# Kernel tuning notes

Hardware: AMD Instinct MI355X
Metric: run time of the kernel (lower is better)

Reference implementation:

```python
import jax, jax.numpy as jnp
import numpy as np

B, K = 2048, 128
M = 5 * K
ALPHA = 1.0 / K          # alpha_k = 1/K
VARTHETA = 0.1
PMAX = 10.0
BIG = 1e9


def _gnn(HW, X, W0a, W1a, W0b, W1b):
    """Order-1 graph filter GNN (HWGCN, K0=[1,1]): relu hidden layer, linear output.
    HW: (B,K,K), X: (B,K,Fin) -> (B,K,Fout)."""
    SX = jnp.einsum('bij,bjf->bif', HW, X)
    Z = jax.nn.relu(X @ W0a + SX @ W1a)              # (B,K,32)
    SZ = jnp.einsum('bij,bjh->bih', HW, Z)
    return Z @ W0b + SZ @ W1b                        # (B,K,Fout)


def setup_inputs() -> dict:
    key = jax.random.key(0)
    ks = jax.random.split(key, 16)
    s = 0.05
    d = {
        'num_itr': 10,
        'kth': 9,
        'HW': jnp.abs(jax.random.normal(ks[0], (B, K, K), jnp.float32)) * s,
        'x0_tmp': jax.random.uniform(ks[1], (B, M), jnp.float32),
        'nu3_val': jnp.array([0.1], jnp.float32),
        'tilde_gamma_val': jnp.array([2.0], jnp.float32),
        'A9': jax.random.normal(ks[2], (1,), jnp.float32),
        'A1': jax.random.normal(ks[3], (1,), jnp.float32),
        'A3': jax.random.normal(ks[4], (1,), jnp.float32),
        'A7': jax.random.normal(ks[5], (1,), jnp.float32),
        'b7': jax.random.normal(ks[6], (1,), jnp.float32),
        'A10': jax.random.normal(ks[7], (1,), jnp.float32),
        'g1_W0a': jax.random.normal(ks[8], (5, 32), jnp.float32) * s,
        'g1_W1a': jax.random.normal(ks[9], (5, 32), jnp.float32) * s,
        'g1_W0b': jax.random.normal(ks[10], (32, 2), jnp.float32) * s,
        'g1_W1b': jax.random.normal(ks[11], (32, 2), jnp.float32) * s,
        'g2_W0a': jax.random.normal(ks[12], (K + 5, 32), jnp.float32) * s,
        'g2_W1a': jax.random.normal(ks[13], (K + 5, 32), jnp.float32) * s,
        'g2_W0b': jax.random.normal(ks[14], (32, 5), jnp.float32) * s,
        'g2_W1b': jax.random.normal(ks[15], (32, 5), jnp.float32) * s,
    }
    return d


def reference(num_itr, kth, HW, x0_tmp, nu3_val, tilde_gamma_val,
              A9, A1, A3, A7, b7, A10,
              g1_W0a, g1_W1a, g1_W0b, g1_W1b,
              g2_W0a, g2_W1a, g2_W0b, g2_W1b):
    nu3 = nu3_val[0]
    tg = tilde_gamma_val[0]
    x = x0_tmp                                        # (B, 5K)

    # REGNN 1 -> step sizes lbd (B,2)
    X1 = x.reshape(B, 5, K).transpose(0, 2, 1)        # (B,K,5)
    lbd = jax.nn.relu(jnp.mean(_gnn(HW, X1, g1_W0a, g1_W1a, g1_W0b, g1_W1b), axis=1))

    # vectorized per-K gradient steps on segments [K:2K] and [4K:5K]
    s0, s1, s2, s3, s4 = (x[:, i * K:(i + 1) * K] for i in range(5))
    s1 = s1 - lbd[:, 0:1] * (ALPHA / (1.0 + s1))
    s4 = s4 + lbd[:, 1:2] * (ALPHA * VARTHETA)
    x = jnp.concatenate([s0, s1, s2, s3, s4], axis=1)

    # REGNN 2 correction
    X2 = x.reshape(B, 5, K).transpose(0, 2, 1)        # (B,K,5)
    tilde = _gnn(HW, jnp.concatenate([HW, X2], axis=-1),
                 g2_W0a, g2_W1a, g2_W0b, g2_W1b)      # (B,K,5)
    x = x + tilde.transpose(0, 2, 1).reshape(B, M)

    # proj onto C8: sum of first K entries <= Pmax (||q||^2 = K)
    f = jnp.sum(x[:, :K], axis=1) - PMAX              # (B,)
    q = jnp.concatenate([jnp.ones(K, x.dtype), jnp.zeros(4 * K, x.dtype)])
    x = jnp.where((f <= 0)[:, None], x, x - f[:, None] * q / K)

    # banded elementwise box clamps (faithful sequential max/min)
    idx = jnp.arange(M)
    band = lambda a, b: (idx >= a) & (idx < b)
    Vnu = 1.0 - 1.0 / (1.0 + nu3) ** 2
    Vg = 1.0 - 1.0 / (1.0 + tg) ** 2
    x = jnp.maximum(jnp.where(band(K, 2 * K), nu3, 0.0), x)
    x = jnp.minimum(jnp.where(band(2 * K, 3 * K), tg, BIG), x)
    x = jnp.maximum(jnp.where(band(3 * K, 4 * K), Vnu, 0.0), x)
    x = jnp.minimum(jnp.where(band(3 * K, 4 * K), Vg, BIG), x)

    if kth == num_itr - 1:  # static python branch
        x = jnp.maximum(x, 0.0)
        xg = x[:, 2 * K:3 * K]   # gamma
        xv = x[:, 3 * K:4 * K]   # V
        f5 = 1.0 - 1.0 / (1.0 + xg) ** 2 - xv
        f6 = jnp.sqrt(xv) - x[:, 4 * K:5 * K]
        p = x[:, 0:K]
        nu = x[:, K:2 * K]
        diagHW = jnp.diagonal(HW, axis1=1, axis2=2)   # (B,K)
        top = p * diagHW
        down = jnp.einsum('bi,bij->bj', p, HW) - top + 1.0
        f4 = top - down * xg
        f2 = nu * down - top
        return (x, f5, f6, f4, f2)
    return (x,)
```

## Files before the change

kernel.cpp:

```cpp
#include <hip/hip_runtime.h>
#include <math.h>

#define B_N 2048
#define KK 128
#define MM 640
#define HS 136
#define ZSS 40
#define SXS 12
#define ALPHA (1.0f/128.0f)
#define VARTHETA 0.1f
#define PMAXV 10.0f
#define BIGV 1000000000.0f

typedef __attribute__((ext_vector_type(8))) short short8;
typedef __attribute__((ext_vector_type(4))) short short4v;
typedef __attribute__((ext_vector_type(4))) float floatx4;
typedef __attribute__((ext_vector_type(4))) __bf16 bf16x4;

static __device__ __forceinline__ unsigned short f2bf(float f) {
    return __builtin_bit_cast(unsigned short, (__bf16)f);
}
static __device__ __forceinline__ short4v cvt4(floatx4 v) {
    return __builtin_bit_cast(short4v, __builtin_convertvector(v, bf16x4));
}
static __device__ __forceinline__ float bf2f(unsigned short h) {
    unsigned u = ((unsigned)h) << 16;
    return __builtin_bit_cast(float, u);
}
static __device__ __forceinline__ short8 pack8(floatx4 lo, floatx4 hi) {
    short4v a = cvt4(lo), b4 = cvt4(hi);
    return __builtin_shufflevector(a, b4, 0, 1, 2, 3, 4, 5, 6, 7);
}

#define POOLA_OFF 0
#define POOLB_OFF 10240
#define POOL_BYTES (10240 + 8704)

__global__ __launch_bounds__(512, 4)
void unfold_pocs_kernel(
    const int* __restrict__ num_itr_p, const int* __restrict__ kth_p,
    const float* __restrict__ HW, const float* __restrict__ x0,
    const float* __restrict__ nu3_p, const float* __restrict__ tg_p,
    const float* __restrict__ g1_W0a, const float* __restrict__ g1_W1a,
    const float* __restrict__ g1_W0b, const float* __restrict__ g1_W1b,
    const float* __restrict__ g2_W0a, const float* __restrict__ g2_W1a,
    const float* __restrict__ g2_W0b, const float* __restrict__ g2_W1b,
    float* __restrict__ out)
{
    __shared__ __align__(16) unsigned char pool[POOL_BYTES];
    __shared__ __align__(16) float xb[MM];
    __shared__ __align__(16) unsigned short xbf[5*HS];
    __shared__ __align__(16) unsigned short x2bf[KK*8];
    __shared__ __align__(16) unsigned short w1abf[32*8];
    __shared__ __align__(16) unsigned short w0abf[32*8];
    __shared__ __align__(16) float g1w0a[160], g1w1a[160];
    __shared__ __align__(16) float g1w0b[64],  g1w1b[64];
    __shared__ __align__(16) float w0b2[160],  w1b2[160];
    __shared__ __align__(16) float cw[8*KK];
    __shared__ float red[16];

    unsigned short* w1aT = (unsigned short*)(pool + POOLA_OFF);
    unsigned short* zbp  = (unsigned short*)(pool + POOLA_OFF);
    float*          SXs  = (float*)(pool + POOLB_OFF);
    unsigned short* c2T  = (unsigned short*)(pool + POOLB_OFF);
    unsigned short* eT   = (unsigned short*)(pool + POOLB_OFF);
    float*          t0f  = (float*)(pool + POOLB_OFF + 2048);

    const int t = threadIdx.x;
    const int b = blockIdx.x;
    const float* HWb = HW + (size_t)b * (KK*KK);

    const int wv = t >> 6, lane = t & 63, quad = lane >> 4, lr = lane & 15;
    const int arow = wv*16 + lr;

    {
        const int n = t & 31, seg = t >> 5;
        unsigned short tmp[8];
        #pragma unroll
        for (int i = 0; i < 8; ++i) tmp[i] = f2bf(g2_W1a[(seg*8 + i)*32 + n]);
        *(short8*)&w1aT[n*HS + seg*8] = *(short8*)tmp;
    }
    {
        const int n = (t & 255) >> 3, j = t & 7;
        if (t < 256) w1abf[t]       = (j < 5) ? f2bf(g2_W1a[(KK + j)*32 + n]) : (unsigned short)0;
        else if (t < 512) w0abf[t - 256] = (j < 5) ? f2bf(g2_W0a[(KK + j)*32 + n]) : (unsigned short)0;
    }
    if (t < 160) {
        floatx4 v = *(const floatx4*)(x0 + (size_t)b*MM + t*4);
        *(floatx4*)(xb + t*4) = v;
        *(short4v*)&xbf[(t >> 5)*HS + ((t*4) & 127)] = cvt4(v);
        g1w0a[t] = g1_W0a[t];
        g1w1a[t] = g1_W1a[t];
        w0b2[t]  = g2_W0b[t];
        w1b2[t]  = g2_W1b[t];
    }
    if (t < 64) { g1w0b[t] = g1_W0b[t]; g1w1b[t] = g1_W1b[t]; }
    __syncthreads();

    short8 A[4];
    #pragma unroll
    for (int kt = 0; kt < 4; ++kt) {
        const float* arp = HWb + arow*KK + kt*32 + quad*8;
        floatx4 lo = *(const floatx4*)(arp);
        floatx4 hi = *(const floatx4*)(arp + 4);
        A[kt] = pack8(lo, hi);
    }

    #pragma unroll
    for (int kt = 0; kt < 4; ++kt) {
        float v[8];
        #pragma unroll
        for (int j = 0; j < 8; ++j) v[j] = bf2f((unsigned short)A[kt][j]);
        #pragma unroll
        for (int s = 1; s < 16; s <<= 1) {
            #pragma unroll
            for (int j = 0; j < 8; ++j) v[j] += __shfl_xor(v[j], s);
        }
        if (lr == 0) {
            #pragma unroll
            for (int j = 0; j < 8; ++j) cw[wv*KK + kt*32 + quad*8 + j] = v[j];
        }
    }

    {
        floatx4 acc = {0.f, 0.f, 0.f, 0.f};
        const int ns = lr < 5 ? lr : 4;
        #pragma unroll
        for (int kt = 0; kt < 4; ++kt) {
            short8 bb = *(const short8*)&xbf[ns*HS + kt*32 + quad*8];
            acc = __builtin_amdgcn_mfma_f32_16x16x32_bf16(A[kt], bb, acc, 0, 0, 0);
        }
        if (lr < 5) {
            #pragma unroll
            for (int r = 0; r < 4; ++r)
                SXs[(wv*16 + quad*4 + r)*SXS + lr] = acc[r];
        }
    }
    __syncthreads();

    const int row = t >> 2, g = t & 3;

    {
        float sx[5], x1r[5];
        #pragma unroll
        for (int f = 0; f < 5; ++f) { sx[f] = SXs[row*SXS + f]; x1r[f] = xb[f*KK + row]; }

        float zb0p0=0, zb0p1=0, zb1p0=0, zb1p1=0;
        #pragma unroll
        for (int hh = 0; hh < 8; ++hh) {
            int h = 8*g + hh;
            float a = 0.0f;
            #pragma unroll
            for (int f = 0; f < 5; ++f) a += x1r[f]*g1w0a[f*32+h] + sx[f]*g1w1a[f*32+h];
            a = fmaxf(a, 0.0f);
            zb0p0 += a * g1w0b[h*2+0];
            zb0p1 += a * g1w0b[h*2+1];
            zb1p0 += a * g1w1b[h*2+0];
            zb1p1 += a * g1w1b[h*2+1];
        }
        float mp = 0.0f;
        #pragma unroll
        for (int w = 0; w < 8; ++w) mp += cw[w*KK + row];
        float m = mp * (1.0f/KK);
        float c0 = zb0p0*(1.0f/KK) + m*zb1p0;
        float c1 = zb0p1*(1.0f/KK) + m*zb1p1;
        #pragma unroll
        for (int s = 1; s < 64; s <<= 1) { c0 += __shfl_xor(c0, s); c1 += __shfl_xor(c1, s); }
        if (lane == 0) { red[wv*2] = c0; red[wv*2 + 1] = c1; }
    }
    __syncthreads();

    {
        float lbd0 = 0.f, lbd1 = 0.f;
        #pragma unroll
        for (int w2 = 0; w2 < 8; ++w2) { lbd0 += red[w2*2]; lbd1 += red[w2*2+1]; }
        lbd0 = fmaxf(lbd0, 0.0f); lbd1 = fmaxf(lbd1, 0.0f);

        const int i0 = 2*t, m = i0 >> 3, f0 = i0 & 7;
        float va = (f0     < 5) ? xb[f0*KK + m]     : 0.f;
        float vb = (f0 + 1 < 5) ? xb[(f0+1)*KK + m] : 0.f;
        if (f0 == 0) { vb = vb - lbd0 * (ALPHA / (1.0f + vb)); xb[KK + m]   = vb; }
        if (f0 == 4) { va = va + lbd1 * (ALPHA * VARTHETA);    xb[4*KK + m] = va; }
        ushort2 p; p.x = f2bf(va); p.y = f2bf(vb);
        *(ushort2*)&x2bf[i0] = p;
    }
    __syncthreads();

    #pragma unroll
    for (int nt = 0; nt < 2; ++nt) {
        const int n = nt*16 + lr, mmb = wv*16 + quad*4;
        floatx4 acc = {0.f, 0.f, 0.f, 0.f};
        short8 ax2 = {0,0,0,0,0,0,0,0}, bx2 = {0,0,0,0,0,0,0,0};
        if (quad == 0) {
            ax2 = *(const short8*)&x2bf[(wv*16 + lr)*8];
            bx2 = *(const short8*)&w1abf[n*8];
        }
        acc = __builtin_amdgcn_mfma_f32_16x16x32_bf16(ax2, bx2, acc, 0, 0, 0);
        #pragma unroll
        for (int kt = 0; kt < 4; ++kt) {
            short8 bb = *(const short8*)&w1aT[n*HS + kt*32 + quad*8];
            acc = __builtin_amdgcn_mfma_f32_16x16x32_bf16(A[kt], bb, acc, 0, 0, 0);
        }
        ushort4 pe;
        pe.x = f2bf(acc[0] + g2_W0a[(mmb+0)*32 + n]);
        pe.y = f2bf(acc[1] + g2_W0a[(mmb+1)*32 + n]);
        pe.z = f2bf(acc[2] + g2_W0a[(mmb+2)*32 + n]);
        pe.w = f2bf(acc[3] + g2_W0a[(mmb+3)*32 + n]);
        *(ushort4*)&c2T[n*HS + mmb] = pe;
    }
    __syncthreads();

    #pragma unroll
    for (int nt = 0; nt < 2; ++nt) {
        const int n = nt*16 + lr, mmb = wv*16 + quad*4;
        floatx4 acc = {0.f, 0.f, 0.f, 0.f};
        short8 ax2 = {0,0,0,0,0,0,0,0}, bx2 = {0,0,0,0,0,0,0,0};
        if (quad == 0) {
            ax2 = *(const short8*)&x2bf[(wv*16 + lr)*8];
            bx2 = *(const short8*)&w0abf[n*8];
        }
        acc = __builtin_amdgcn_mfma_f32_16x16x32_bf16(ax2, bx2, acc, 0, 0, 0);
        #pragma unroll
        for (int kt = 0; kt < 4; ++kt) {
            short8 bb = *(const short8*)&c2T[n*HS + kt*32 + quad*8];
            acc = __builtin_amdgcn_mfma_f32_16x16x32_bf16(A[kt], bb, acc, 0, 0, 0);
        }
        #pragma unroll
        for (int r = 0; r < 4; ++r)
            zbp[(mmb + r)*ZSS + n] = f2bf(fmaxf(acc[r], 0.0f));
    }
    __syncthreads();

    {
        float ev[5] = {0,0,0,0,0}, t0v[5] = {0,0,0,0,0};
        short8 zrow = *(const short8*)&zbp[row*ZSS + g*8];
        #pragma unroll
        for (int hh = 0; hh < 8; ++hh) {
            int h = 8*g + hh;
            float zv = bf2f((unsigned short)zrow[hh]);
            #pragma unroll
            for (int c = 0; c < 5; ++c) {
                ev[c]  += zv * w1b2[h*5 + c];
                t0v[c] += zv * w0b2[h*5 + c];
            }
        }
        #pragma unroll
        for (int c = 0; c < 5; ++c) {
            ev[c]  += __shfl_xor(ev[c], 1);  ev[c]  += __shfl_xor(ev[c], 2);
            t0v[c] += __shfl_xor(t0v[c], 1); t0v[c] += __shfl_xor(t0v[c], 2);
        }
        if (g == 0) {
            #pragma unroll
            for (int c = 0; c < 5; ++c) {
                eT[c*HS + row]  = f2bf(ev[c]);
                t0f[row*8 + c]  = t0v[c];
            }
        }
    }
    __syncthreads();

    {
        floatx4 acc = {0.f, 0.f, 0.f, 0.f};
        const int ns = lr < 5 ? lr : 4;
        #pragma unroll
        for (int kt = 0; kt < 4; ++kt) {
            short8 bb = *(const short8*)&eT[ns*HS + kt*32 + quad*8];
            acc = __builtin_amdgcn_mfma_f32_16x16x32_bf16(A[kt], bb, acc, 0, 0, 0);
        }
        if (lr < 5) {
            #pragma unroll
            for (int r = 0; r < 4; ++r) {
                int mm = wv*16 + quad*4 + r;
                xb[lr*KK + mm] += acc[r] + t0f[mm*8 + lr];
            }
        }
    }
    __syncthreads();

    float pv = (t < KK) ? xb[t] : 0.0f;
    #pragma unroll
    for (int s = 1; s < 64; s <<= 1) pv += __shfl_xor(pv, s);
    if (lane == 0) red[wv] = pv;
    __syncthreads();
    float fv = -PMAXV;
    #pragma unroll
    for (int w2 = 0; w2 < 8; ++w2) fv += red[w2];

    const int num_itr = num_itr_p[0], kth = kth_p[0];
    const bool flag = (kth == num_itr - 1);
    const float nu3 = nu3_p[0], tg = tg_p[0];
    const float onu = 1.0f + nu3, otg = 1.0f + tg;
    const float Vnu = 1.0f - 1.0f/(onu*onu), Vg = 1.0f - 1.0f/(otg*otg);
    float* outx = out + (size_t)b * MM;

    #pragma unroll
    for (int r2 = 0; r2 < 2; ++r2) {
        int idx = r2*512 + t;
        if (idx < MM) {
            float v = xb[idx];
            if (idx < KK && fv > 0.0f) v -= fv * (1.0f/KK);
            v = fmaxf(v, (idx >= KK   && idx < 2*KK) ? nu3 : 0.0f);
            v = fminf(v, (idx >= 2*KK && idx < 3*KK) ? tg  : BIGV);
            v = fmaxf(v, (idx >= 3*KK && idx < 4*KK) ? Vnu : 0.0f);
            v = fminf(v, (idx >= 3*KK && idx < 4*KK) ? Vg  : BIGV);
            if (flag) v = fmaxf(v, 0.0f);
            xb[idx] = v;
            outx[idx] = v;
        }
    }

    if (flag) {
        __syncthreads();
        const size_t O1 = (size_t)B_N*MM;
        const size_t OK = (size_t)B_N*KK;
        if (t < KK) {
            float xg = xb[2*KK + t], xv = xb[3*KK + t];
            float u1 = 1.0f + xg;
            out[O1 + (size_t)b*KK + t]      = 1.0f - 1.0f/(u1*u1) - xv;
            out[O1 + OK + (size_t)b*KK + t] = sqrtf(xv) - xb[4*KK + t];
        }
        {
            float pval = xb[arow];
            #pragma unroll
            for (int kt = 0; kt < 4; ++kt) {
                float v[8];
                #pragma unroll
                for (int j = 0; j < 8; ++j) v[j] = pval * bf2f((unsigned short)A[kt][j]);
                #pragma unroll
                for (int s = 1; s < 16; s <<= 1) {
                    #pragma unroll
                    for (int j = 0; j < 8; ++j) v[j] += __shfl_xor(v[j], s);
                }
                if (lr == 0) {
                    #pragma unroll
                    for (int j = 0; j < 8; ++j) cw[wv*KK + kt*32 + quad*8 + j] = v[j];
                }
            }
        }
        __syncthreads();
        if (t < KK) {
            float dp = 0.0f;
            #pragma unroll
            for (int w = 0; w < 8; ++w) dp += cw[w*KK + t];
            float p_  = xb[t], nuv = xb[KK + t], xg = xb[2*KK + t];
            float diag = bf2f(f2bf(HWb[t*KK + t]));
            float top  = p_ * diag;
            float down = dp - top + 1.0f;
            out[O1 + 2*OK + (size_t)b*KK + t] = top - down * xg;
            out[O1 + 3*OK + (size_t)b*KK + t] = nuv * down - top;
        }
    }
}

extern "C" void kernel_launch(void* const* d_in, const int* in_sizes, int n_in,
                              void* d_out, int out_size, void* d_ws, size_t ws_size,
                              hipStream_t stream) {
    unfold_pocs_kernel<<<dim3(B_N), dim3(512), 0, stream>>>(
        (const int*)d_in[0], (const int*)d_in[1],
        (const float*)d_in[2], (const float*)d_in[3],
        (const float*)d_in[4], (const float*)d_in[5],
        (const float*)d_in[12], (const float*)d_in[13],
        (const float*)d_in[14], (const float*)d_in[15],
        (const float*)d_in[16], (const float*)d_in[17],
        (const float*)d_in[18], (const float*)d_in[19],
        (float*)d_out);
}
```

Baseline: 295.8 us.

## Stage HW tile in LDS as bf16 and compute column sums from shared memory

The per-block HW matrix is now loaded cooperatively into a bf16 LDS tile. The MFMA A-fragments are read from that tile instead of being kept in registers from the start, and the column-mean reduction reads LDS columns directly instead of doing a shuffle tree. The final-iteration HW pass reloads from global memory through a laundered pointer so the compiler does not keep A live across the kernel. Launch bounds rise to 6 blocks per CU, trading a larger LDS footprint (about 35KB H tile) against fewer live registers and less shuffle work.

```diff
diff --git a/kernel.cpp b/kernel.cpp
--- a/kernel.cpp
+++ b/kernel.cpp
@@ -31,12 +31,19 @@
     short4v a = cvt4(lo), b4 = cvt4(hi);
     return __builtin_shufflevector(a, b4, 0, 1, 2, 3, 4, 5, 6, 7);
 }
-
-#define POOLA_OFF 0
-#define POOLB_OFF 10240
-#define POOL_BYTES (10240 + 8704)
-
-__global__ __launch_bounds__(512, 4)
+static __device__ __forceinline__ const float* launder_ptr(const float* p) {
+    unsigned long long v = (unsigned long long)p;
+    asm volatile("" : "+s"(v));
+    return (const float*)v;
+}
+
+#define H_W1AT 0
+#define H_C2T  8704
+#define H_ZBP  17408
+#define H_ET   27648
+#define H_T0F  29696
+
+__global__ __launch_bounds__(512, 6)
 void unfold_pocs_kernel(
     const int* __restrict__ num_itr_p, const int* __restrict__ kth_p,
     const float* __restrict__ HW, const float* __restrict__ x0,
@@ -47,7 +54,8 @@
     const float* __restrict__ g2_W0b, const float* __restrict__ g2_W1b,
     float* __restrict__ out)
 {
-    __shared__ __align__(16) unsigned char pool[POOL_BYTES];
+    __shared__ __align__(16) unsigned char H[KK*HS*2];
+    __shared__ __align__(16) float SXs_s[KK*SXS];
     __shared__ __align__(16) float xb[MM];
     __shared__ __align__(16) unsigned short xbf[5*HS];
     __shared__ __align__(16) unsigned short x2bf[KK*8];
@@ -56,15 +64,16 @@
     __shared__ __align__(16) float g1w0a[160], g1w1a[160];
     __shared__ __align__(16) float g1w0b[64],  g1w1b[64];
     __shared__ __align__(16) float w0b2[160],  w1b2[160];
-    __shared__ __align__(16) float cw[8*KK];
     __shared__ float red[16];
 
-    unsigned short* w1aT = (unsigned short*)(pool + POOLA_OFF);
-    unsigned short* zbp  = (unsigned short*)(pool + POOLA_OFF);
-    float*          SXs  = (float*)(pool + POOLB_OFF);
-    unsigned short* c2T  = (unsigned short*)(pool + POOLB_OFF);
-    unsigned short* eT   = (unsigned short*)(pool + POOLB_OFF);
-    float*          t0f  = (float*)(pool + POOLB_OFF + 2048);
+    unsigned short* hwb  = (unsigned short*)H;
+    unsigned short* w1aT = (unsigned short*)(H + H_W1AT);
+    unsigned short* c2T  = (unsigned short*)(H + H_C2T);
+    unsigned short* zbp  = (unsigned short*)(H + H_ZBP);
+    unsigned short* eT   = (unsigned short*)(H + H_ET);
+    float*          t0f  = (float*)(H + H_T0F);
+    float*          cw   = (float*)H;
+    float*          SXs  = SXs_s;
 
     const int t = threadIdx.x;
     const int b = blockIdx.x;
@@ -73,12 +82,12 @@
     const int wv = t >> 6, lane = t & 63, quad = lane >> 4, lr = lane & 15;
     const int arow = wv*16 + lr;
 
-    {
-        const int n = t & 31, seg = t >> 5;
-        unsigned short tmp[8];
-        #pragma unroll
-        for (int i = 0; i < 8; ++i) tmp[i] = f2bf(g2_W1a[(seg*8 + i)*32 + n]);
-        *(short8*)&w1aT[n*HS + seg*8] = *(short8*)tmp;
+    #pragma unroll
+    for (int it = 0; it < 8; ++it) {
+        int qi = it * 512 + t;
+        int rrow = qi >> 5, q = qi & 31;
+        floatx4 v = *(const floatx4*)(HWb + rrow*KK + q*4);
+        *(short4v*)&hwb[rrow*HS + q*4] = cvt4(v);
     }
     {
         const int n = (t & 255) >> 3, j = t & 7;
@@ -97,38 +106,14 @@
     if (t < 64) { g1w0b[t] = g1_W0b[t]; g1w1b[t] = g1_W1b[t]; }
     __syncthreads();
 
-    short8 A[4];
-    #pragma unroll
-    for (int kt = 0; kt < 4; ++kt) {
-        const float* arp = HWb + arow*KK + kt*32 + quad*8;
-        floatx4 lo = *(const floatx4*)(arp);
-        floatx4 hi = *(const floatx4*)(arp + 4);
-        A[kt] = pack8(lo, hi);
-    }
-
-    #pragma unroll
-    for (int kt = 0; kt < 4; ++kt) {
-        float v[8];
-        #pragma unroll
-        for (int j = 0; j < 8; ++j) v[j] = bf2f((unsigned short)A[kt][j]);
-        #pragma unroll
-        for (int s = 1; s < 16; s <<= 1) {
-            #pragma unroll
-            for (int j = 0; j < 8; ++j) v[j] += __shfl_xor(v[j], s);
-        }
-        if (lr == 0) {
-            #pragma unroll
-            for (int j = 0; j < 8; ++j) cw[wv*KK + kt*32 + quad*8 + j] = v[j];
-        }
-    }
-
     {
         floatx4 acc = {0.f, 0.f, 0.f, 0.f};
         const int ns = lr < 5 ? lr : 4;
         #pragma unroll
         for (int kt = 0; kt < 4; ++kt) {
-            short8 bb = *(const short8*)&xbf[ns*HS + kt*32 + quad*8];
-            acc = __builtin_amdgcn_mfma_f32_16x16x32_bf16(A[kt], bb, acc, 0, 0, 0);
+            short8 a  = *(const short8*)&hwb[arow*HS + kt*32 + quad*8];
+            short8 bb = *(const short8*)&xbf[ns*HS   + kt*32 + quad*8];
+            acc = __builtin_amdgcn_mfma_f32_16x16x32_bf16(a, bb, acc, 0, 0, 0);
         }
         if (lr < 5) {
             #pragma unroll
@@ -140,6 +125,7 @@
 
     const int row = t >> 2, g = t & 3;
 
+    short8 A[4];
     {
         float sx[5], x1r[5];
         #pragma unroll
@@ -159,8 +145,11 @@
             zb1p1 += a * g1w1b[h*2+1];
         }
         float mp = 0.0f;
-        #pragma unroll
-        for (int w = 0; w < 8; ++w) mp += cw[w*KK + row];
+        for (int w = 0; w < 32; ++w) {
+            int i = 4*w + g;
+            mp += bf2f(hwb[i*HS + row]);
+        }
+        mp += __shfl_xor(mp, 1); mp += __shfl_xor(mp, 2);
         float m = mp * (1.0f/KK);
         float c0 = zb0p0*(1.0f/KK) + m*zb1p0;
         float c1 = zb0p1*(1.0f/KK) + m*zb1p1;
@@ -168,6 +157,9 @@
         for (int s = 1; s < 64; s <<= 1) { c0 += __shfl_xor(c0, s); c1 += __shfl_xor(c1, s); }
         if (lane == 0) { red[wv*2] = c0; red[wv*2 + 1] = c1; }
     }
+    #pragma unroll
+    for (int kt = 0; kt < 4; ++kt)
+        A[kt] = *(const short8*)&hwb[arow*HS + kt*32 + quad*8];
     __syncthreads();
 
     {
@@ -183,6 +175,13 @@
         if (f0 == 4) { va = va + lbd1 * (ALPHA * VARTHETA);    xb[4*KK + m] = va; }
         ushort2 p; p.x = f2bf(va); p.y = f2bf(vb);
         *(ushort2*)&x2bf[i0] = p;
+    }
+    {
+        const int n = t & 31, seg = t >> 5;
+        unsigned short tmp[8];
+        #pragma unroll
+        for (int i = 0; i < 8; ++i) tmp[i] = f2bf(g2_W1a[(seg*8 + i)*32 + n]);
+        *(short8*)&w1aT[n*HS + seg*8] = *(short8*)tmp;
     }
     __syncthreads();
 
@@ -320,12 +319,17 @@
             out[O1 + OK + (size_t)b*KK + t] = sqrtf(xv) - xb[4*KK + t];
         }
         {
+            const float* hwr = launder_ptr(HWb);
             float pval = xb[arow];
             #pragma unroll
             for (int kt = 0; kt < 4; ++kt) {
+                const float* arp = hwr + arow*KK + kt*32 + quad*8;
+                floatx4 lo = *(const floatx4*)(arp);
+                floatx4 hi = *(const floatx4*)(arp + 4);
+                short8 ad = pack8(lo, hi);
                 float v[8];
                 #pragma unroll
-                for (int j = 0; j < 8; ++j) v[j] = pval * bf2f((unsigned short)A[kt][j]);
+                for (int j = 0; j < 8; ++j) v[j] = pval * bf2f((unsigned short)ad[j]);
                 #pragma unroll
                 for (int s = 1; s < 16; s <<= 1) {
                     #pragma unroll
```

Result: faster. 264.5 us (-10.6%).
